# Performance work log

Measured on AMD Instinct MI355X. Metric: run time of the kernel, lower is better.

## Reference

```python
import jax, jax.numpy as jnp
import numpy as np
from jax.scipy.special import logsumexp

_INF = 1e8
_GAMMA_MIN = 1e-4


def _cosine_cost(x, y):
    # 1 - cosine similarity, batched: [B,M,D] x [B,N,D] -> [B,M,N]
    xn = x / jnp.clip(jnp.linalg.norm(x, axis=-1, keepdims=True), 1e-8)
    yn = y / jnp.clip(jnp.linalg.norm(y, axis=-1, keepdims=True), 1e-8)
    return 1.0 - jnp.einsum('bmd,bnd->bmn', xn, yn)


def _soft_dtw_alignment(cost, gv):
    B, M, N = cost.shape
    dt = cost.dtype
    ii = jnp.arange(M)          # full diagonal index range, masked per step

    # ---- forward DP: R[b, i+1, j+1] = C[i,j] + softmin(R[i,j], R[i,j+1], R[i+1,j]) ----
    R0 = jnp.full((B, M + 1, N + 1), _INF, dtype=dt).at[:, 0, 0].set(0.0)

    def fstep(R, d):
        jj = d - ii
        valid = (jj >= 0) & (jj < N)            # (M,)
        jjc = jnp.clip(jj, 0, N - 1)
        ip, jp = ii + 1, jjc + 1
        p = jnp.stack([R[:, ip - 1, jp - 1],
                       R[:, ip - 1, jp],
                       R[:, ip, jp - 1]], axis=-1)          # (B, M, 3)
        soft = -gv * logsumexp(p / -gv, axis=-1)            # soft-min
        new = cost[:, ii, jjc] + soft                       # (B, M)
        cur = R[:, ip, jp]
        R = R.at[:, ip, jp].set(jnp.where(valid[None, :], new, cur))
        return R, None

    R, _ = jax.lax.scan(fstep, R0, jnp.arange(M + N - 1))
    distance = R[:, M, N]

    # ---- backward DP for alignment matrix E ----
    E0 = jnp.zeros((B, M + 2, N + 2), dtype=dt).at[:, M, N].set(1.0)
    Re = jnp.full((B, M + 2, N + 2), -_INF, dtype=dt).at[:, :M + 1, :N + 1].set(R)
    Ce = jnp.zeros((B, M + 2, N + 2), dtype=dt).at[:, 1:M + 1, 1:N + 1].set(cost)

    def bstep(E, d):
        jj = d - ii
        valid = (jj >= 0) & (jj < N)
        jjc = jnp.clip(jj, 0, N - 1)
        ip, jp = ii + 1, jjc + 1
        rc = Re[:, ip, jp]
        wd = jnp.exp(jnp.clip((Re[:, ip + 1, jp + 1] - Ce[:, ip + 1, jp + 1] - rc) / gv, -50, 50))
        wn = jnp.exp(jnp.clip((Re[:, ip + 1, jp] - Ce[:, ip + 1, jp] - rc) / gv, -50, 50))
        wr = jnp.exp(jnp.clip((Re[:, ip, jp + 1] - Ce[:, ip, jp + 1] - rc) / gv, -50, 50))
        new = E[:, ip + 1, jp + 1] * wd + E[:, ip + 1, jp] * wn + E[:, ip, jp + 1] * wr
        cur = E[:, ip, jp]
        E = E.at[:, ip, jp].set(jnp.where(valid[None, :], new, cur))
        return E, None

    E, _ = jax.lax.scan(bstep, E0, jnp.arange(M + N - 3, -1, -1))
    alignment = E[:, 1:M + 1, 1:N + 1]
    return alignment, distance


def setup_inputs() -> dict:
    key = jax.random.key(0)
    k1, k2 = jax.random.split(key)
    B, M, N, D = 8, 256, 256, 512
    x = jax.random.normal(k1, (B, M, D), dtype=jnp.float32)
    y = jax.random.normal(k2, (B, N, D), dtype=jnp.float32)
    gamma = jnp.asarray(1.0, dtype=jnp.float32)   # learned nn.Parameter
    return {"x": x, "y": y, "gamma": gamma}


def reference(x, y, gamma):
    cost = _cosine_cost(x, y)
    gv = jnp.maximum(jnp.abs(gamma), _GAMMA_MIN)   # effective gamma
    alignment, distance = _soft_dtw_alignment(cost, gv)
    return alignment, distance
```

## Files before the change

kernel.cpp:

```cpp
#include <hip/hip_runtime.h>

#define USTR 192

#define EXP2F(x) __builtin_amdgcn_exp2f(x)
#define LOG2F(x) __builtin_amdgcn_logf(x)

__device__ __forceinline__ void ld4(float d[4], const float* p) {
  float4 v = *(const float4*)p;
  d[0] = v.x; d[1] = v.y; d[2] = v.z; d[3] = v.w;
}

__global__ void __launch_bounds__(256) norms_kernel(const float* __restrict__ x,
                                                    const float* __restrict__ y,
                                                    float* __restrict__ rnx,
                                                    float* __restrict__ rny) {
  int g = blockIdx.x * 4 + (threadIdx.x >> 6);
  int lane = threadIdx.x & 63;
  const float* src; float* dst; int row;
  if (g < 2048) { src = x; dst = rnx; row = g; }
  else          { src = y; dst = rny; row = g - 2048; }
  const float* p = src + (size_t)row * 512;
  float4 v0 = *(const float4*)(p + lane * 4);
  float4 v1 = *(const float4*)(p + 256 + lane * 4);
  float s = v0.x*v0.x + v0.y*v0.y + v0.z*v0.z + v0.w*v0.w
          + v1.x*v1.x + v1.y*v1.y + v1.z*v1.z + v1.w*v1.w;
#pragma unroll
  for (int o = 32; o > 0; o >>= 1) s += __shfl_xor(s, o, 64);
  if (lane == 0) dst[row] = 1.0f / fmaxf(sqrtf(s), 1e-8f);
}

__global__ void __launch_bounds__(256) cost_gemm(const float* __restrict__ x,
                                                 const float* __restrict__ y,
                                                 const float* __restrict__ rnx,
                                                 const float* __restrict__ rny,
                                                 const float* __restrict__ gamma,
                                                 float* __restrict__ mAll) {
  int b = blockIdx.z, mt = blockIdx.y, nt = blockIdx.x;
  int m0 = mt * 32, n0 = nt * 64;
  __shared__ float Xs[16][36];
  __shared__ float Ys[16][68];
  int tid = threadIdx.x;
  int row = tid >> 2, cq = tid & 3;
  int tx = tid & 15, ty = tid >> 4;
  const float* xb = x + ((size_t)b * 256 + m0) * 512;
  const float* yb = y + ((size_t)b * 256 + n0) * 512;
  float acc[2][4] = {};
  for (int k0 = 0; k0 < 512; k0 += 16) {
    float4 xv;
    if (tid < 128) xv = *(const float4*)(xb + (size_t)row * 512 + k0 + cq * 4);
    float4 yv = *(const float4*)(yb + (size_t)row * 512 + k0 + cq * 4);
    __syncthreads();
    if (tid < 128) {
      Xs[cq*4+0][row] = xv.x; Xs[cq*4+1][row] = xv.y;
      Xs[cq*4+2][row] = xv.z; Xs[cq*4+3][row] = xv.w;
    }
    Ys[cq*4+0][row] = yv.x; Ys[cq*4+1][row] = yv.y;
    Ys[cq*4+2][row] = yv.z; Ys[cq*4+3][row] = yv.w;
    __syncthreads();
#pragma unroll
    for (int kk = 0; kk < 16; ++kk) {
      float a0 = Xs[kk][ty * 2 + 0];
      float a1 = Xs[kk][ty * 2 + 1];
      float4 bv = *(const float4*)(&Ys[kk][tx * 4]);
      float br[4] = {bv.x, bv.y, bv.z, bv.w};
#pragma unroll
      for (int c = 0; c < 4; ++c) {
        acc[0][c] += a0 * br[c];
        acc[1][c] += a1 * br[c];
      }
    }
  }
  float gv = fmaxf(fabsf(gamma[0]), 1e-4f);
  float ig2 = 1.4426950408889634f / gv;
  float rx[2], ry[4];
#pragma unroll
  for (int r = 0; r < 2; ++r) rx[r] = rnx[b * 256 + m0 + ty * 2 + r];
#pragma unroll
  for (int c = 0; c < 4; ++c) ry[c] = rny[b * 256 + n0 + tx * 4 + c];
  int l = nt * 16 + tx;
  int v = mt * 16 + ty;
  int u = v + l;
  float4 stm[2];
#pragma unroll
  for (int r = 0; r < 2; ++r) {
    float c0 = (1.0f - acc[r][0] * rx[r] * ry[0]) * ig2;
    float c1 = (1.0f - acc[r][1] * rx[r] * ry[1]) * ig2;
    float c2 = (1.0f - acc[r][2] * rx[r] * ry[2]) * ig2;
    float c3 = (1.0f - acc[r][3] * rx[r] * ry[3]) * ig2;
    stm[r] = (float4){EXP2F(-c0), EXP2F(-c1), EXP2F(-c2), EXP2F(-c3)};
  }
  float* mpF = mAll + ((size_t)b * USTR + u) * 512 + l * 8;
  *(float4*)(mpF)     = stm[0];
  *(float4*)(mpF + 4) = stm[1];
  float* mpR = mAll + ((size_t)(8 + b) * USTR + (190 - u)) * 512 + (63 - l) * 8;
  *(float4*)(mpR)     = (float4){stm[1].w, stm[1].z, stm[1].y, stm[1].x};
  *(float4*)(mpR + 4) = (float4){stm[0].w, stm[0].z, stm[0].y, stm[0].x};
}

__global__ void __launch_bounds__(64, 1) pass_kernel(const float* __restrict__ mAll,
                                                     float* __restrict__ pAll,
                                                     float* __restrict__ QepAll,
                                                     const float* __restrict__ gamma,
                                                     float* __restrict__ dist_out) {
  int blk = blockIdx.x, l = threadIdx.x;
  int dir = blk >> 3, b = blk & 7;
  float gv = fmaxf(fabsf(gamma[0]), 1e-4f);
  float gl = gv * 0.6931471805599453f;
  const float* mb = mAll + (size_t)blk * USTR * 512 + l * 8;
  float* pb = pAll + (size_t)blk * USTR * 512 + l * 8;
  float* qe = QepAll + ((size_t)blk * 64 + l) * 24;
  float Pp0 = 0.f, Pp1 = 0.f, Pp2 = 0.f, Pp3 = 0.f;
  float bot0 = 0.f, bot1 = 0.f;
  int Q = 0;
  float ucar = (l == 0) ? 1.0f : 0.f;
  float A0[8], A1[8], A2[8], A3[8], A4[8], A5[8], A6[8], A7[8];
  float A8[8], A9[8], A10[8], A11[8], A12[8], A13[8], A14[8], A15[8];
  auto loadC = [&](int t, float* buf) {
    int u = t > 190 ? 190 : t;
    const float* p = mb + (size_t)u * 512;
    ld4(buf, p); ld4(buf + 4, p + 4);
  };
  auto body = [&](int t, const float* mm) {
    bool act = (unsigned)(t - l) <= 127u;
    float s0 = __shfl_up(bot0, 1);
    float s1 = __shfl_up(bot1, 1);
    int  liQ = __shfl_up(Q, 1);
    if (l == 0) { s0 = 0.f; s1 = 0.f; }
    else { int adj = liQ - Q; s0 = ldexpf(s0, adj); s1 = ldexpf(s1, adj); }
    float v0 = mm[0] * (Pp0 + s0 + ucar);
    float v1 = mm[1] * (Pp1 + v0 + Pp0);
    float v2 = mm[2] * (Pp2 + v1 + Pp1);
    float v3 = mm[3] * (Pp3 + v2 + Pp2);
    float w0 = mm[4] * (v0 + s1 + s0);
    float w1 = mm[5] * (v1 + w0 + v0);
    float w2 = mm[6] * (v2 + w1 + v1);
    float w3 = mm[7] * (v3 + w2 + v2);
    if (act) {
      float* sp = pb + (size_t)t * 512;
      *(float4*)(sp)     = (float4){v0, v1, v2, v3};
      *(float4*)(sp + 4) = (float4){w0, w1, w2, w3};
      Pp0 = w0; Pp1 = w1; Pp2 = w2; Pp3 = w3;
      ucar = s1; bot0 = v3; bot1 = w3;
      if (dir == 0 && l == 63 && t == 190)
        dist_out[b] = (-(float)Q - LOG2F(w3)) * gl;
    }
  };
  auto renorm = [&](int tEnd) {
    if ((unsigned)(tEnd - l) <= 127u) {
      int e = (int)((__float_as_uint(Pp3) >> 23) & 255u) - 127;
      Pp0 = ldexpf(Pp0, -e); Pp1 = ldexpf(Pp1, -e);
      Pp2 = ldexpf(Pp2, -e); Pp3 = ldexpf(Pp3, -e);
      ucar = ldexpf(ucar, -e);
      bot0 = ldexpf(bot0, -e); bot1 = ldexpf(bot1, -e);
      Q += e;
    }
  };
  loadC(0, A0);  loadC(1, A1);  loadC(2, A2);  loadC(3, A3);
  loadC(4, A4);  loadC(5, A5);  loadC(6, A6);  loadC(7, A7);
  loadC(8, A8);  loadC(9, A9);  loadC(10, A10); loadC(11, A11);
  loadC(12, A12); loadC(13, A13); loadC(14, A14); loadC(15, A15);
  for (int it = 0; it < 12; ++it) {
    int s = it * 16;
    qe[2 * it] = (float)Q;
    body(s + 0, A0); loadC(s + 16, A0);
    body(s + 1, A1); loadC(s + 17, A1);
    body(s + 2, A2); loadC(s + 18, A2);
    body(s + 3, A3); loadC(s + 19, A3);
    body(s + 4, A4); loadC(s + 20, A4);
    body(s + 5, A5); loadC(s + 21, A5);
    body(s + 6, A6); loadC(s + 22, A6);
    body(s + 7, A7); loadC(s + 23, A7);
    renorm(s + 7);
    qe[2 * it + 1] = (float)Q;
    body(s + 8,  A8);  loadC(s + 24, A8);
    body(s + 9,  A9);  loadC(s + 25, A9);
    body(s + 10, A10); loadC(s + 26, A10);
    body(s + 11, A11); loadC(s + 27, A11);
    body(s + 12, A12); loadC(s + 28, A12);
    body(s + 13, A13); loadC(s + 29, A13);
    body(s + 14, A14); loadC(s + 30, A14);
    body(s + 15, A15); loadC(s + 31, A15);
    renorm(s + 15);
  }
}

__global__ void __launch_bounds__(256) e_kernel(const float* __restrict__ mAll,
                                                const float* __restrict__ pAll,
                                                const float* __restrict__ QepAll,
                                                float* __restrict__ out) {
  int tid = blockIdx.x * 256 + threadIdx.x;
  int l = tid & 63;
  int r = (tid >> 6) & 255;
  int b = tid >> 14;
  int v = r >> 1, rf = r & 1;
  int uF = v + l;
  int uR = 190 - v - l;
  const float* pF  = pAll + ((size_t)b * USTR + uF) * 512 + l * 8 + rf * 4;
  const float* pRv = pAll + ((size_t)(8 + b) * USTR + uR) * 512 + (63 - l) * 8 + (1 - rf) * 4;
  const float* mF  = mAll + ((size_t)b * USTR + uF) * 512 + l * 8 + rf * 4;
  float P[4], Bv[4], M[4];
  ld4(P, pF); ld4(Bv, pRv); ld4(M, mF);
  float Qf = QepAll[((size_t)b * 64 + l) * 24 + (uF >> 3)];
  float Qb = QepAll[((size_t)(8 + b) * 64 + (63 - l)) * 24 + (uR >> 3)];
  float Zp = pAll[((size_t)b * USTR + 190) * 512 + 511];
  float Zq = QepAll[((size_t)b * 64 + 63) * 24 + 23];
  int e = (int)(Qf + Qb - Zq);
  float inv = 1.0f / Zp;
  float4 o;
  o.x = ldexpf(P[0] * Bv[3] / M[0] * inv, e);
  o.y = ldexpf(P[1] * Bv[2] / M[1] * inv, e);
  o.z = ldexpf(P[2] * Bv[1] / M[2] * inv, e);
  o.w = ldexpf(P[3] * Bv[0] / M[3] * inv, e);
  *(float4*)(out + (size_t)b * 65536 + (size_t)r * 256 + 4 * l) = o;
}

extern "C" void kernel_launch(void* const* d_in, const int* in_sizes, int n_in,
                              void* d_out, int out_size, void* d_ws, size_t ws_size,
                              hipStream_t stream) {
  const float* x = (const float*)d_in[0];
  const float* y = (const float*)d_in[1];
  const float* gamma = (const float*)d_in[2];
  float* out = (float*)d_out;
  float* ws = (float*)d_ws;

  const size_t PMAT = (size_t)16 * USTR * 512;
  float* rnx    = ws;
  float* rny    = ws + 2048;
  float* mAll   = ws + 4096;
  float* pAll   = mAll + PMAT;
  float* QepAll = pAll + PMAT;

  norms_kernel<<<1024, 256, 0, stream>>>(x, y, rnx, rny);
  cost_gemm<<<dim3(4, 8, 8), 256, 0, stream>>>(x, y, rnx, rny, gamma, mAll);
  pass_kernel<<<16, 64, 0, stream>>>(mAll, pAll, QepAll, gamma, out + 524288);
  e_kernel<<<512, 256, 0, stream>>>(mAll, pAll, QepAll, out);
}
```

Measured before the change: 125.5 us.

## Fuse row norms into cost GEMM and drop reversed cost matrix copy

```diff
diff --git a/kernel.cpp b/kernel.cpp
--- a/kernel.cpp
+++ b/kernel.cpp
@@ -10,29 +10,8 @@
   d[0] = v.x; d[1] = v.y; d[2] = v.z; d[3] = v.w;
 }
 
-__global__ void __launch_bounds__(256) norms_kernel(const float* __restrict__ x,
-                                                    const float* __restrict__ y,
-                                                    float* __restrict__ rnx,
-                                                    float* __restrict__ rny) {
-  int g = blockIdx.x * 4 + (threadIdx.x >> 6);
-  int lane = threadIdx.x & 63;
-  const float* src; float* dst; int row;
-  if (g < 2048) { src = x; dst = rnx; row = g; }
-  else          { src = y; dst = rny; row = g - 2048; }
-  const float* p = src + (size_t)row * 512;
-  float4 v0 = *(const float4*)(p + lane * 4);
-  float4 v1 = *(const float4*)(p + 256 + lane * 4);
-  float s = v0.x*v0.x + v0.y*v0.y + v0.z*v0.z + v0.w*v0.w
-          + v1.x*v1.x + v1.y*v1.y + v1.z*v1.z + v1.w*v1.w;
-#pragma unroll
-  for (int o = 32; o > 0; o >>= 1) s += __shfl_xor(s, o, 64);
-  if (lane == 0) dst[row] = 1.0f / fmaxf(sqrtf(s), 1e-8f);
-}
-
 __global__ void __launch_bounds__(256) cost_gemm(const float* __restrict__ x,
                                                  const float* __restrict__ y,
-                                                 const float* __restrict__ rnx,
-                                                 const float* __restrict__ rny,
                                                  const float* __restrict__ gamma,
                                                  float* __restrict__ mAll) {
   int b = blockIdx.z, mt = blockIdx.y, nt = blockIdx.x;
@@ -45,10 +24,15 @@
   const float* xb = x + ((size_t)b * 256 + m0) * 512;
   const float* yb = y + ((size_t)b * 256 + n0) * 512;
   float acc[2][4] = {};
+  float px = 0.f, py = 0.f;
   for (int k0 = 0; k0 < 512; k0 += 16) {
     float4 xv;
-    if (tid < 128) xv = *(const float4*)(xb + (size_t)row * 512 + k0 + cq * 4);
+    if (tid < 128) {
+      xv = *(const float4*)(xb + (size_t)row * 512 + k0 + cq * 4);
+      px += xv.x*xv.x + xv.y*xv.y + xv.z*xv.z + xv.w*xv.w;
+    }
     float4 yv = *(const float4*)(yb + (size_t)row * 512 + k0 + cq * 4);
+    py += yv.x*yv.x + yv.y*yv.y + yv.z*yv.z + yv.w*yv.w;
     __syncthreads();
     if (tid < 128) {
       Xs[cq*4+0][row] = xv.x; Xs[cq*4+1][row] = xv.y;
@@ -70,31 +54,40 @@
       }
     }
   }
+  __syncthreads();
+  float* xsf = &Xs[0][0];
+  float* ysf = &Ys[0][0];
+  if (tid < 128) xsf[tid] = px;
+  ysf[tid] = py;
+  __syncthreads();
+  float rx[2], ry[4];
+#pragma unroll
+  for (int r = 0; r < 2; ++r) {
+    int lr = ty * 2 + r;
+    float s = xsf[lr*4] + xsf[lr*4+1] + xsf[lr*4+2] + xsf[lr*4+3];
+    rx[r] = 1.0f / fmaxf(sqrtf(s), 1e-8f);
+  }
+#pragma unroll
+  for (int c = 0; c < 4; ++c) {
+    int lc = tx * 4 + c;
+    float s = ysf[lc*4] + ysf[lc*4+1] + ysf[lc*4+2] + ysf[lc*4+3];
+    ry[c] = 1.0f / fmaxf(sqrtf(s), 1e-8f);
+  }
   float gv = fmaxf(fabsf(gamma[0]), 1e-4f);
   float ig2 = 1.4426950408889634f / gv;
-  float rx[2], ry[4];
-#pragma unroll
-  for (int r = 0; r < 2; ++r) rx[r] = rnx[b * 256 + m0 + ty * 2 + r];
-#pragma unroll
-  for (int c = 0; c < 4; ++c) ry[c] = rny[b * 256 + n0 + tx * 4 + c];
   int l = nt * 16 + tx;
   int v = mt * 16 + ty;
   int u = v + l;
-  float4 stm[2];
+  float* mp = mAll + ((size_t)b * USTR + u) * 512 + l * 8;
 #pragma unroll
   for (int r = 0; r < 2; ++r) {
     float c0 = (1.0f - acc[r][0] * rx[r] * ry[0]) * ig2;
     float c1 = (1.0f - acc[r][1] * rx[r] * ry[1]) * ig2;
     float c2 = (1.0f - acc[r][2] * rx[r] * ry[2]) * ig2;
     float c3 = (1.0f - acc[r][3] * rx[r] * ry[3]) * ig2;
-    stm[r] = (float4){EXP2F(-c0), EXP2F(-c1), EXP2F(-c2), EXP2F(-c3)};
-  }
-  float* mpF = mAll + ((size_t)b * USTR + u) * 512 + l * 8;
-  *(float4*)(mpF)     = stm[0];
-  *(float4*)(mpF + 4) = stm[1];
-  float* mpR = mAll + ((size_t)(8 + b) * USTR + (190 - u)) * 512 + (63 - l) * 8;
-  *(float4*)(mpR)     = (float4){stm[1].w, stm[1].z, stm[1].y, stm[1].x};
-  *(float4*)(mpR + 4) = (float4){stm[0].w, stm[0].z, stm[0].y, stm[0].x};
+    float4 stm = {EXP2F(-c0), EXP2F(-c1), EXP2F(-c2), EXP2F(-c3)};
+    *(float4*)(mp + 4 * r) = stm;
+  }
 }
 
 __global__ void __launch_bounds__(64, 1) pass_kernel(const float* __restrict__ mAll,
@@ -104,11 +97,13 @@
                                                      float* __restrict__ dist_out) {
   int blk = blockIdx.x, l = threadIdx.x;
   int dir = blk >> 3, b = blk & 7;
+  bool rev = (dir == 1);
   float gv = fmaxf(fabsf(gamma[0]), 1e-4f);
   float gl = gv * 0.6931471805599453f;
-  const float* mb = mAll + (size_t)blk * USTR * 512 + l * 8;
-  float* pb = pAll + (size_t)blk * USTR * 512 + l * 8;
+  const float* mb = mAll + (size_t)b * USTR * 512;
+  float* pb = pAll + (size_t)blk * USTR * 512;
   float* qe = QepAll + ((size_t)blk * 64 + l) * 24;
+  int lOff = rev ? (63 - l) * 8 : l * 8;
   float Pp0 = 0.f, Pp1 = 0.f, Pp2 = 0.f, Pp3 = 0.f;
   float bot0 = 0.f, bot1 = 0.f;
   int Q = 0;
@@ -116,9 +111,18 @@
   float A0[8], A1[8], A2[8], A3[8], A4[8], A5[8], A6[8], A7[8];
   float A8[8], A9[8], A10[8], A11[8], A12[8], A13[8], A14[8], A15[8];
   auto loadC = [&](int t, float* buf) {
-    int u = t > 190 ? 190 : t;
-    const float* p = mb + (size_t)u * 512;
-    ld4(buf, p); ld4(buf + 4, p + 4);
+    int tc = t > 190 ? 190 : t;
+    int u = rev ? (190 - tc) : tc;
+    const float* p = mb + (size_t)u * 512 + lOff;
+    float tmp[8];
+    ld4(tmp, p); ld4(tmp + 4, p + 4);
+    if (rev) {
+#pragma unroll
+      for (int j = 0; j < 8; ++j) buf[j] = tmp[7 - j];
+    } else {
+#pragma unroll
+      for (int j = 0; j < 8; ++j) buf[j] = tmp[j];
+    }
   };
   auto body = [&](int t, const float* mm) {
     bool act = (unsigned)(t - l) <= 127u;
@@ -136,13 +140,19 @@
     float w2 = mm[6] * (v2 + w1 + v1);
     float w3 = mm[7] * (v3 + w2 + v2);
     if (act) {
-      float* sp = pb + (size_t)t * 512;
-      *(float4*)(sp)     = (float4){v0, v1, v2, v3};
-      *(float4*)(sp + 4) = (float4){w0, w1, w2, w3};
+      if (!rev) {
+        float* sp = pb + (size_t)t * 512 + lOff;
+        *(float4*)(sp)     = (float4){v0, v1, v2, v3};
+        *(float4*)(sp + 4) = (float4){w0, w1, w2, w3};
+        if (l == 63 && t == 190)
+          dist_out[b] = (-(float)Q - LOG2F(w3)) * gl;
+      } else {
+        float* sp = pb + (size_t)(190 - t) * 512 + lOff;
+        *(float4*)(sp)     = (float4){w3, w2, w1, w0};
+        *(float4*)(sp + 4) = (float4){v3, v2, v1, v0};
+      }
       Pp0 = w0; Pp1 = w1; Pp2 = w2; Pp3 = w3;
       ucar = s1; bot0 = v3; bot1 = w3;
-      if (dir == 0 && l == 63 && t == 190)
-        dist_out[b] = (-(float)Q - LOG2F(w3)) * gl;
     }
   };
   auto renorm = [&](int tEnd) {
@@ -194,23 +204,23 @@
   int b = tid >> 14;
   int v = r >> 1, rf = r & 1;
   int uF = v + l;
-  int uR = 190 - v - l;
-  const float* pF  = pAll + ((size_t)b * USTR + uF) * 512 + l * 8 + rf * 4;
-  const float* pRv = pAll + ((size_t)(8 + b) * USTR + uR) * 512 + (63 - l) * 8 + (1 - rf) * 4;
-  const float* mF  = mAll + ((size_t)b * USTR + uF) * 512 + l * 8 + rf * 4;
+  size_t off = ((size_t)uF * 512) + l * 8 + rf * 4;
+  const float* pF = pAll + (size_t)b * USTR * 512 + off;
+  const float* pB = pAll + (size_t)(8 + b) * USTR * 512 + off;
+  const float* mF = mAll + (size_t)b * USTR * 512 + off;
   float P[4], Bv[4], M[4];
-  ld4(P, pF); ld4(Bv, pRv); ld4(M, mF);
+  ld4(P, pF); ld4(Bv, pB); ld4(M, mF);
   float Qf = QepAll[((size_t)b * 64 + l) * 24 + (uF >> 3)];
-  float Qb = QepAll[((size_t)(8 + b) * 64 + (63 - l)) * 24 + (uR >> 3)];
-  float Zp = pAll[((size_t)b * USTR + 190) * 512 + 511];
+  float Qb = QepAll[((size_t)(8 + b) * 64 + (63 - l)) * 24 + ((190 - uF) >> 3)];
+  float Zp = pAll[((size_t)b * USTR + 190) * 512 + 63 * 8 + 7];
   float Zq = QepAll[((size_t)b * 64 + 63) * 24 + 23];
   int e = (int)(Qf + Qb - Zq);
   float inv = 1.0f / Zp;
   float4 o;
-  o.x = ldexpf(P[0] * Bv[3] / M[0] * inv, e);
-  o.y = ldexpf(P[1] * Bv[2] / M[1] * inv, e);
-  o.z = ldexpf(P[2] * Bv[1] / M[2] * inv, e);
-  o.w = ldexpf(P[3] * Bv[0] / M[3] * inv, e);
+  o.x = ldexpf(P[0] * Bv[0] / M[0] * inv, e);
+  o.y = ldexpf(P[1] * Bv[1] / M[1] * inv, e);
+  o.z = ldexpf(P[2] * Bv[2] / M[2] * inv, e);
+  o.w = ldexpf(P[3] * Bv[3] / M[3] * inv, e);
   *(float4*)(out + (size_t)b * 65536 + (size_t)r * 256 + 4 * l) = o;
 }
 
@@ -223,15 +233,11 @@
   float* out = (float*)d_out;
   float* ws = (float*)d_ws;
 
-  const size_t PMAT = (size_t)16 * USTR * 512;
-  float* rnx    = ws;
-  float* rny    = ws + 2048;
-  float* mAll   = ws + 4096;
-  float* pAll   = mAll + PMAT;
-  float* QepAll = pAll + PMAT;
-
-  norms_kernel<<<1024, 256, 0, stream>>>(x, y, rnx, rny);
-  cost_gemm<<<dim3(4, 8, 8), 256, 0, stream>>>(x, y, rnx, rny, gamma, mAll);
+  float* mAll   = ws;
+  float* pAll   = mAll + (size_t)8 * USTR * 512;
+  float* QepAll = pAll + (size_t)16 * USTR * 512;
+
+  cost_gemm<<<dim3(4, 8, 8), 256, 0, stream>>>(x, y, gamma, mAll);
   pass_kernel<<<16, 64, 0, stream>>>(mAll, pAll, QepAll, gamma, out + 524288);
   e_kernel<<<512, 256, 0, stream>>>(mAll, pAll, QepAll, out);
 }
```

After: 148.0 us. 17.9% more time.
